# Performance work log

Measured on AMD Instinct MI355X. Metric: run time of the kernel, lower is better.

Reference implementation:

```python
import jax, jax.numpy as jnp
import numpy as np

NUM_LAYER = 5
EMB = 300
FEAT = 512
NUM_GRAPHS = 64
BN_EPS = 1e-5


def setup_inputs() -> dict:
    key = jax.random.key(0)
    ks = jax.random.split(key, 32)
    N, E = 16000, 256000
    x = jax.random.randint(ks[0], (N, 2), 0, 3)  # col0: atom type (<119), col1: chirality (<3)
    edge_index = jax.random.randint(ks[1], (2, E), 0, N)
    edge_attr = jax.random.randint(ks[2], (E, 2), 0, 3)  # col0: bond type (<6), col1: direction (<3)
    batch = jnp.sort(jax.random.randint(ks[3], (N,), 0, NUM_GRAPHS))

    def xav(k, shape):
        fan_in, fan_out = shape[-2], shape[-1]
        lim = float(np.sqrt(6.0 / (fan_in + fan_out)))
        return jax.random.uniform(k, shape, jnp.float32, -lim, lim)

    inp = dict(x=x, edge_index=edge_index, edge_attr=edge_attr, batch=batch)
    inp['x_emb1'] = xav(ks[4], (119, EMB))
    inp['x_emb2'] = xav(ks[5], (3, EMB))
    inp['e1_emb'] = xav(ks[6], (NUM_LAYER, 6, EMB))
    inp['e2_emb'] = xav(ks[7], (NUM_LAYER, 3, EMB))
    inp['w1'] = xav(ks[8], (NUM_LAYER, EMB, 2 * EMB))
    inp['b1'] = jnp.zeros((NUM_LAYER, 2 * EMB))
    inp['w2'] = xav(ks[9], (NUM_LAYER, 2 * EMB, EMB))
    inp['b2'] = jnp.zeros((NUM_LAYER, EMB))
    inp['bn_g'] = jnp.ones((NUM_LAYER, EMB))
    inp['bn_b'] = jnp.zeros((NUM_LAYER, EMB))
    inp['feat_w'] = xav(ks[10], (EMB, FEAT))
    inp['feat_b'] = jnp.zeros((FEAT,))
    inp['hw1'] = xav(ks[11], (FEAT, FEAT // 2))
    inp['hb1'] = jnp.zeros((FEAT // 2,))
    inp['hw2'] = xav(ks[12], (FEAT // 2, FEAT // 2))
    inp['hb2'] = jnp.zeros((FEAT // 2,))
    inp['hw3'] = xav(ks[13], (FEAT // 2, 2))
    inp['hb3'] = jnp.zeros((2,))
    return inp


def gin_forward(x, edge_index, edge_attr, batch,
                x_emb1, x_emb2, e1_emb, e2_emb, w1, b1, w2, b2,
                bn_g, bn_b, feat_w, feat_b, hw1, hb1, hw2, hb2, hw3, hb3):
    N = x.shape[0]
    h = x_emb1[x[:, 0]] + x_emb2[x[:, 1]]  # [N, EMB]
    # add self-loops once (same for every layer): attr = (5, 0)
    loops = jnp.broadcast_to(jnp.arange(N)[None, :], (2, N))
    ei = jnp.concatenate([edge_index, loops], axis=1)  # [2, E+N]
    loop_attr = jnp.concatenate([jnp.full((N, 1), 5, edge_attr.dtype),
                                 jnp.zeros((N, 1), edge_attr.dtype)], axis=1)
    ea = jnp.concatenate([edge_attr, loop_attr], axis=0)  # [E+N, 2]
    src, dst = ei[0], ei[1]
    for l in range(NUM_LAYER):
        edge_emb = e1_emb[l][ea[:, 0]] + e2_emb[l][ea[:, 1]]  # [E+N, EMB]
        msg = h[src] + edge_emb
        agg = jax.ops.segment_sum(msg, dst, num_segments=N)  # scatter-add
        h = jax.nn.relu(agg @ w1[l] + b1[l]) @ w2[l] + b2[l]  # GIN MLP update
        mean = jnp.mean(h, axis=0)
        var = jnp.var(h, axis=0)
        h = (h - mean) * jax.lax.rsqrt(var + BN_EPS) * bn_g[l] + bn_b[l]
        if l < NUM_LAYER - 1:
            h = jax.nn.relu(h)
    # global mean pool per graph
    sums = jax.ops.segment_sum(h, batch, num_segments=NUM_GRAPHS)
    cnts = jax.ops.segment_sum(jnp.ones((N,), h.dtype), batch, num_segments=NUM_GRAPHS)
    hg = sums / jnp.maximum(cnts, 1.0)[:, None]  # [G, EMB]
    hf = hg @ feat_w + feat_b  # [G, FEAT]
    p = jax.nn.softplus(hf @ hw1 + hb1)
    p = jax.nn.softplus(p @ hw2 + hb2)
    pred = p @ hw3 + hb3  # [G, 2]
    return hf, pred


def reference(x, edge_index, edge_attr, batch,
              x_emb1, x_emb2, e1_emb, e2_emb, w1, b1, w2, b2,
              bn_g, bn_b, feat_w, feat_b, hw1, hb1, hw2, hb2, hw3, hb3):
    return gin_forward(x, edge_index, edge_attr, batch,
                       x_emb1, x_emb2, e1_emb, e2_emb, w1, b1, w2, b2,
                       bn_g, bn_b, feat_w, feat_b, hw1, hb1, hw2, hb2, hw3, hb3)
```

## Files before the change

kernel.cpp:

```cpp
#include <hip/hip_runtime.h>

#define NODES 16000
#define EDGES 256000
#define ETOT  272000
#define EMB   300
#define KP1   320
#define NP1   640
#define NP2B  384
#define NGRAPH 64
#define LAYERS 5
#define INV_N (1.0f / 16000.0f)

typedef unsigned short u16;
typedef unsigned int u32;
typedef __bf16 bf16_t;
typedef bf16_t bf16x8 __attribute__((ext_vector_type(8)));
typedef float f32x4 __attribute__((ext_vector_type(4)));

__device__ inline u16 f2bf(float f) {
    bf16_t b = (bf16_t)f;
    return __builtin_bit_cast(u16, b);
}
__device__ inline float bf_lo(u32 u) { return __builtin_bit_cast(float, u << 16); }
__device__ inline float bf_hi(u32 u) { return __builtin_bit_cast(float, u & 0xFFFF0000u); }
__device__ inline u32 bf_pack(float lo, float hi) {
    return ((u32)f2bf(hi) << 16) | (u32)f2bf(lo);
}

__device__ inline float softplus_f(float x) {
    return fmaxf(x, 0.f) + log1pf(expf(-fabsf(x)));
}

__device__ inline void gload_lds16(const u16* g, u16* l) {
    __builtin_amdgcn_global_load_lds(
        (const __attribute__((address_space(1))) void*)g,
        (__attribute__((address_space(3))) void*)l, 16, 0, 0);
}

__device__ inline void bn_coef(const float* __restrict__ ssum, const float* __restrict__ ssq,
                               const float* __restrict__ g, const float* __restrict__ b,
                               int c, float& s, float& t) {
    float mean = ssum[c] * INV_N;
    float var = ssq[c] * INV_N - mean * mean;
    float rstd = rsqrtf(var + 1e-5f);
    s = rstd * g[c];
    t = b[c] - mean * s;
}

__global__ void k_count(const int* __restrict__ ei, int* __restrict__ cnt) {
    int e = blockIdx.x * 256 + threadIdx.x;
    if (e >= ETOT) return;
    int dst = (e < EDGES) ? ei[EDGES + e] : (e - EDGES);
    atomicAdd(&cnt[dst], 1);
}

__global__ void k_scan(const int* cnt_in, int* row_off, int* cursor) {
    __shared__ int s[1024];
    __shared__ int carry;
    int t = threadIdx.x;
    if (t == 0) { carry = 0; row_off[0] = 0; }
    __syncthreads();
    for (int base = 0; base < NODES; base += 1024) {
        int idx = base + t;
        int v = (idx < NODES) ? cnt_in[idx] : 0;
        s[t] = v;
        __syncthreads();
        for (int off = 1; off < 1024; off <<= 1) {
            int add = (t >= off) ? s[t - off] : 0;
            __syncthreads();
            s[t] += add;
            __syncthreads();
        }
        int incl = s[t];
        int c = carry;
        if (idx < NODES) { row_off[idx + 1] = c + incl; cursor[idx] = c + incl - v; }
        __syncthreads();
        if (t == 1023) carry = c + incl;
        __syncthreads();
    }
}

__global__ void k_fill(const int* __restrict__ ei, const int* __restrict__ ea,
                       int* __restrict__ cursor, int* __restrict__ packed) {
    int e = blockIdx.x * 256 + threadIdx.x;
    if (e >= ETOT) return;
    int src, dst, c;
    if (e < EDGES) {
        src = ei[e]; dst = ei[EDGES + e];
        c = ea[e * 2] * 3 + ea[e * 2 + 1];
    } else {
        src = dst = e - EDGES; c = 15;
    }
    int pos = atomicAdd(&cursor[dst], 1);
    packed[pos] = src | (c << 20);
}

__global__ void k_embed(const int* __restrict__ x, const float* __restrict__ e1,
                        const float* __restrict__ e2, u16* __restrict__ h) {
    int id = blockIdx.x * 256 + threadIdx.x;
    if (id >= NODES * EMB) return;
    int i = id / EMB, f = id - i * EMB;
    h[id] = f2bf(e1[x[2 * i] * EMB + f] + e2[x[2 * i + 1] * EMB + f]);
}

__global__ void k_comb(const float* __restrict__ e1, const float* __restrict__ e2,
                       u16* __restrict__ comb) {
    int id = blockIdx.x * 256 + threadIdx.x;
    if (id >= LAYERS * 18 * EMB) return;
    int l = id / (18 * EMB);
    int r = id - l * 18 * EMB;
    int c = r / EMB, f = r - c * EMB;
    int a = c / 3, b = c - a * 3;
    comb[id] = f2bf(e1[(l * 6 + a) * EMB + f] + e2[(l * 3 + b) * EMB + f]);
}

__global__ void k_convw1(const float* __restrict__ w1, u16* __restrict__ w1bT) {
    int id = blockIdx.x * 256 + threadIdx.x;
    if (id >= LAYERS * NP1 * KP1) return;
    int l = id / (NP1 * KP1);
    int r = id - l * NP1 * KP1;
    int n = r / KP1, k = r - n * KP1;
    float v = (n < 600 && k < EMB) ? w1[(l * EMB + k) * 600 + n] : 0.f;
    w1bT[id] = f2bf(v);
}

__global__ void k_convw2(const float* __restrict__ w2, u16* __restrict__ w2bT) {
    int id = blockIdx.x * 256 + threadIdx.x;
    if (id >= LAYERS * NP2B * NP1) return;
    int l = id / (NP2B * NP1);
    int r = id - l * NP2B * NP1;
    int n = r / NP1, k = r - n * NP1;
    float v = (n < EMB && k < 600) ? w2[(l * 600 + k) * EMB + n] : 0.f;
    w2bT[id] = f2bf(v);
}

#define AGG_LOAD(P)                                             \
    int pk = packed[P];                                         \
    const u32* hr = hu + (size_t)(pk & 0xFFFFF) * 150;          \
    const u32* cr = cu + (pk >> 20) * 150;                      \
    u32 u0 = hr[lane], u1 = hr[64 + lane];                      \
    u32 v0 = cr[lane], v1 = cr[64 + lane];                      \
    u32 u2 = 0, v2 = 0;                                         \
    if (has2) { u2 = hr[128 + lane]; v2 = cr[128 + lane]; }

#define AGG_BN_ACC()                                            \
    a0l += fmaxf(bf_lo(u0) * s0l + t0l, 0.f) + bf_lo(v0);       \
    a0h += fmaxf(bf_hi(u0) * s0h + t0h, 0.f) + bf_hi(v0);       \
    a1l += fmaxf(bf_lo(u1) * s1l + t1l, 0.f) + bf_lo(v1);       \
    a1h += fmaxf(bf_hi(u1) * s1h + t1h, 0.f) + bf_hi(v1);       \
    a2l += fmaxf(bf_lo(u2) * s2l + t2l, 0.f) + bf_lo(v2);       \
    a2h += fmaxf(bf_hi(u2) * s2h + t2h, 0.f) + bf_hi(v2);

#define AGG_ACC()                                               \
    a0l += bf_lo(u0) + bf_lo(v0);                               \
    a0h += bf_hi(u0) + bf_hi(v0);                               \
    a1l += bf_lo(u1) + bf_lo(v1);                               \
    a1h += bf_hi(u1) + bf_hi(v1);                               \
    a2l += bf_lo(u2) + bf_lo(v2);                               \
    a2h += bf_hi(u2) + bf_hi(v2);

__global__ __launch_bounds__(256) void k_aggregate(
    const u16* __restrict__ h, const int* __restrict__ row_off,
    const int* __restrict__ packed, const u16* __restrict__ comb,
    u16* __restrict__ aggB,
    const float* __restrict__ ssum, const float* __restrict__ ssq,
    const float* __restrict__ bng, const float* __restrict__ bnb, int use_bn) {
    int node = blockIdx.x * 4 + (threadIdx.x >> 6);
    int lane = threadIdx.x & 63;
    int s = row_off[node], e = row_off[node + 1];
    bool has2 = lane < 22;
    const u32* hu = (const u32*)h;
    const u32* cu = (const u32*)comb;
    float s0l = 1.f, t0l = 0.f, s0h = 1.f, t0h = 0.f;
    float s1l = 1.f, t1l = 0.f, s1h = 1.f, t1h = 0.f;
    float s2l = 1.f, t2l = 0.f, s2h = 1.f, t2h = 0.f;
    if (use_bn) {
        bn_coef(ssum, ssq, bng, bnb, 2 * lane,           s0l, t0l);
        bn_coef(ssum, ssq, bng, bnb, 2 * lane + 1,       s0h, t0h);
        bn_coef(ssum, ssq, bng, bnb, 128 + 2 * lane,     s1l, t1l);
        bn_coef(ssum, ssq, bng, bnb, 128 + 2 * lane + 1, s1h, t1h);
        if (has2) {
            bn_coef(ssum, ssq, bng, bnb, 256 + 2 * lane,     s2l, t2l);
            bn_coef(ssum, ssq, bng, bnb, 256 + 2 * lane + 1, s2h, t2h);
        }
    }
    float a0l = 0, a0h = 0, a1l = 0, a1h = 0, a2l = 0, a2h = 0;
    int p = s;
    if (use_bn) {
        for (; p + 1 < e; p += 2) {
            { AGG_LOAD(p); AGG_BN_ACC(); }
            { AGG_LOAD(p + 1); AGG_BN_ACC(); }
        }
        if (p < e) { AGG_LOAD(p); AGG_BN_ACC(); }
    } else {
        for (; p + 1 < e; p += 2) {
            { AGG_LOAD(p); AGG_ACC(); }
            { AGG_LOAD(p + 1); AGG_ACC(); }
        }
        if (p < e) { AGG_LOAD(p); AGG_ACC(); }
    }
    u32* o = (u32*)(aggB + (size_t)node * KP1);
    o[lane] = bf_pack(a0l, a0h);
    o[64 + lane] = bf_pack(a1l, a1h);
    if (lane < 32) o[128 + lane] = has2 ? bf_pack(a2l, a2h) : 0u;
}

template <int MODE>
__global__ __launch_bounds__(256) void k_gemm(
    const u16* __restrict__ A, const u16* __restrict__ Bt,
    const float* __restrict__ bias, int nbias,
    u16* __restrict__ Cv, int ldc, int K,
    float* __restrict__ ssum, float* __restrict__ ssq) {
    __shared__ __align__(16) u16 Al[128 * 32];
    __shared__ __align__(16) u16 Bl[128 * 32];
    __shared__ float rs[2][128];
    __shared__ float rq[2][128];
    int t = threadIdx.x;
    int n0 = blockIdx.x * 128, m0 = blockIdx.y * 128;
    int lane = t & 63, w = t >> 6;
    int wr = w >> 1, wc = w & 1;
    int lr = lane >> 2, lc = lane & 3;
    const u16* gA0 = A + (size_t)(m0 + w * 32 + lr) * K + lc * 8;
    const u16* gA1 = gA0 + (size_t)16 * K;
    const u16* gB0 = Bt + (size_t)(n0 + w * 32 + lr) * K + lc * 8;
    const u16* gB1 = gB0 + (size_t)16 * K;
    u16* lA0 = &Al[(w * 32) * 32];
    u16* lA1 = &Al[(w * 32 + 16) * 32];
    u16* lB0 = &Bl[(w * 32) * 32];
    u16* lB1 = &Bl[(w * 32 + 16) * 32];
    f32x4 acc[4][4];
#pragma unroll
    for (int i = 0; i < 4; i++)
#pragma unroll
        for (int j = 0; j < 4; j++) acc[i][j] = (f32x4){0.f, 0.f, 0.f, 0.f};
    int fr = lane & 15;
    int k0 = (lane >> 4) * 8;
    int abase = (wr * 64 + fr) * 32 + k0;
    int bbase = (wc * 64 + fr) * 32 + k0;
    for (int kt = 0; kt < K; kt += 32) {
        if (kt) __syncthreads();
        gload_lds16(gA0 + kt, lA0);
        gload_lds16(gA1 + kt, lA1);
        gload_lds16(gB0 + kt, lB0);
        gload_lds16(gB1 + kt, lB1);
        __syncthreads();
        bf16x8 af[4], bfv[4];
#pragma unroll
        for (int f = 0; f < 4; ++f) {
            af[f]  = *reinterpret_cast<const bf16x8*>(&Al[abase + f * 16 * 32]);
            bfv[f] = *reinterpret_cast<const bf16x8*>(&Bl[bbase + f * 16 * 32]);
        }
#pragma unroll
        for (int fm = 0; fm < 4; ++fm)
#pragma unroll
            for (int fn = 0; fn < 4; ++fn)
                acc[fm][fn] = __builtin_amdgcn_mfma_f32_16x16x32_bf16(
                    af[fm], bfv[fn], acc[fm][fn], 0, 0, 0);
    }
    int rg = lane >> 4;
    if (MODE == 0) {
#pragma unroll
        for (int fn = 0; fn < 4; ++fn) {
            int col = n0 + wc * 64 + fn * 16 + fr;
            float bv = (col < nbias) ? bias[col] : 0.f;
#pragma unroll
            for (int fm = 0; fm < 4; ++fm) {
                int rb = m0 + wr * 64 + fm * 16 + rg * 4;
#pragma unroll
                for (int j = 0; j < 4; ++j) {
                    float v = fmaxf(acc[fm][fn][j] + bv, 0.f);
                    Cv[(size_t)(rb + j) * ldc + col] = f2bf(v);
                }
            }
        }
    } else {
#pragma unroll
        for (int fn = 0; fn < 4; ++fn) {
            int col = n0 + wc * 64 + fn * 16 + fr;
            float bv = (col < nbias) ? bias[col] : 0.f;
            float cs = 0.f, cq = 0.f;
#pragma unroll
            for (int fm = 0; fm < 4; ++fm) {
                int rb = m0 + wr * 64 + fm * 16 + rg * 4;
#pragma unroll
                for (int j = 0; j < 4; ++j) {
                    float v = acc[fm][fn][j] + bv;
                    if (col < EMB) Cv[(size_t)(rb + j) * EMB + col] = f2bf(v);
                    cs += v;
                    cq += v * v;
                }
            }
            cs += __shfl_xor(cs, 16); cs += __shfl_xor(cs, 32);
            cq += __shfl_xor(cq, 16); cq += __shfl_xor(cq, 32);
            if (rg == 0) {
                rs[wr][wc * 64 + fn * 16 + fr] = cs;
                rq[wr][wc * 64 + fn * 16 + fr] = cq;
            }
        }
        __syncthreads();
        if (t < 128) {
            int col = n0 + t;
            if (col < EMB) {
                atomicAdd(&ssum[col], rs[0][t] + rs[1][t]);
                atomicAdd(&ssq[col], rq[0][t] + rq[1][t]);
            }
        }
    }
}

__global__ void k_goff(const int* __restrict__ batch, int* __restrict__ goff) {
    int t = threadIdx.x;
    if (t > NGRAPH) return;
    int lo = 0, hi = NODES;
    while (lo < hi) { int mid = (lo + hi) >> 1; if (batch[mid] < t) lo = mid + 1; else hi = mid; }
    goff[t] = lo;
}

__global__ __launch_bounds__(256) void k_pool(const u16* __restrict__ h,
                                              const int* __restrict__ goff,
                                              const float* __restrict__ ssum,
                                              const float* __restrict__ ssq,
                                              const float* __restrict__ bng,
                                              const float* __restrict__ bnb,
                                              float* __restrict__ hg) {
    __shared__ float red[4][64];
    int g = blockIdx.x;
    int col = blockIdx.y * 64 + (threadIdx.x & 63);
    int w = threadIdx.x >> 6;
    int s = goff[g], e = goff[g + 1];
    float a = 0.f;
    bool ok = col < EMB;
    if (ok) {
        for (int r = s + w; r < e; r += 4)
            a += __builtin_bit_cast(float, (u32)h[(size_t)r * EMB + col] << 16);
    }
    red[w][threadIdx.x & 63] = a;
    __syncthreads();
    if (w == 0 && ok) {
        float sc, tc;
        bn_coef(ssum, ssq, bng, bnb, col, sc, tc);
        float v = red[0][threadIdx.x] + red[1][threadIdx.x] +
                  red[2][threadIdx.x] + red[3][threadIdx.x];
        float inv = (e > s) ? 1.0f / (float)(e - s) : 0.f;
        hg[(size_t)g * EMB + col] = (v * inv) * sc + tc;
    }
}

template <int ACT>
__global__ __launch_bounds__(256) void k_small_mm(
    const float* __restrict__ A, const float* __restrict__ W,
    const float* __restrict__ bias, float* __restrict__ C, int N, int K) {
    __shared__ float red[4][64];
    int row = blockIdx.x;
    int lane = threadIdx.x & 63;
    int col = blockIdx.y * 64 + lane;
    int w = threadIdx.x >> 6;
    const float* a = A + (size_t)row * K;
    float acc = 0.f;
#pragma unroll 4
    for (int k = w; k < K; k += 4) acc += a[k] * W[(size_t)k * N + col];
    red[w][lane] = acc;
    __syncthreads();
    if (w == 0) {
        float v = red[0][lane] + red[1][lane] + red[2][lane] + red[3][lane] + bias[col];
        if (ACT) v = softplus_f(v);
        C[(size_t)row * N + col] = v;
    }
}

__global__ __launch_bounds__(256) void k_pred(const float* __restrict__ P,
                                              const float* __restrict__ hw3,
                                              const float* __restrict__ hb3,
                                              float* __restrict__ out) {
    __shared__ float red[2][4];
    int g = blockIdx.x;
    int t = threadIdx.x;
    float q = P[(size_t)g * 256 + t];
    float r0 = q * hw3[t * 2 + 0];
    float r1 = q * hw3[t * 2 + 1];
#pragma unroll
    for (int off = 32; off > 0; off >>= 1) {
        r0 += __shfl_down(r0, off);
        r1 += __shfl_down(r1, off);
    }
    if ((t & 63) == 0) { red[0][t >> 6] = r0; red[1][t >> 6] = r1; }
    __syncthreads();
    if (t == 0) {
        out[(size_t)NGRAPH * 512 + g * 2 + 0] = red[0][0] + red[0][1] + red[0][2] + red[0][3] + hb3[0];
        out[(size_t)NGRAPH * 512 + g * 2 + 1] = red[1][0] + red[1][1] + red[1][2] + red[1][3] + hb3[1];
    }
}

extern "C" void kernel_launch(void* const* d_in, const int* in_sizes, int n_in,
                              void* d_out, int out_size, void* d_ws, size_t ws_size,
                              hipStream_t stream) {
    const int* x      = (const int*)d_in[0];
    const int* ei     = (const int*)d_in[1];
    const int* ea     = (const int*)d_in[2];
    const int* batch  = (const int*)d_in[3];
    const float* x_emb1 = (const float*)d_in[4];
    const float* x_emb2 = (const float*)d_in[5];
    const float* e1_emb = (const float*)d_in[6];
    const float* e2_emb = (const float*)d_in[7];
    const float* w1   = (const float*)d_in[8];
    const float* b1   = (const float*)d_in[9];
    const float* w2   = (const float*)d_in[10];
    const float* b2   = (const float*)d_in[11];
    const float* bn_g = (const float*)d_in[12];
    const float* bn_b = (const float*)d_in[13];
    const float* feat_w = (const float*)d_in[14];
    const float* feat_b = (const float*)d_in[15];
    const float* hw1  = (const float*)d_in[16];
    const float* hb1  = (const float*)d_in[17];
    const float* hw2  = (const float*)d_in[18];
    const float* hb2  = (const float*)d_in[19];
    const float* hw3  = (const float*)d_in[20];
    const float* hb3  = (const float*)d_in[21];
    float* out = (float*)d_out;

    char* p = (char*)d_ws;
    auto alloc = [&](size_t bytes) -> char* {
        char* r = p;
        p += ((bytes + 255) / 256) * 256;
        return r;
    };
    u16* h_a     = (u16*)alloc((size_t)NODES * EMB * 2);
    u16* h_b     = (u16*)alloc((size_t)NODES * EMB * 2);
    u16* aggB    = (u16*)alloc((size_t)NODES * KP1 * 2);
    u16* T       = (u16*)alloc((size_t)NODES * NP1 * 2);
    u16* w1bT    = (u16*)alloc((size_t)LAYERS * NP1 * KP1 * 2);
    u16* w2bT    = (u16*)alloc((size_t)LAYERS * NP2B * NP1 * 2);
    u16* comb    = (u16*)alloc((size_t)LAYERS * 18 * EMB * 2);
    int* row_off = (int*)alloc((NODES + 1) * 4);
    int* cursor  = (int*)alloc(NODES * 4);
    int* packed  = (int*)alloc((size_t)ETOT * 4);
    float* stats = (float*)alloc(2 * 304 * 4);
    int* goff    = (int*)alloc((NGRAPH + 1) * 4);
    float* hg    = (float*)alloc((size_t)NGRAPH * EMB * 4);
    float* pb1   = (float*)alloc((size_t)NGRAPH * 256 * 4);
    float* pb2   = (float*)alloc((size_t)NGRAPH * 256 * 4);
    if ((size_t)(p - (char*)d_ws) > ws_size) return;

    float* ssum = stats;
    float* ssq  = stats + 304;

    hipMemsetAsync(cursor, 0, NODES * 4, stream);
    k_count<<<(ETOT + 255) / 256, 256, 0, stream>>>(ei, cursor);
    k_scan<<<1, 1024, 0, stream>>>(cursor, row_off, cursor);
    k_fill<<<(ETOT + 255) / 256, 256, 0, stream>>>(ei, ea, cursor, packed);

    k_embed<<<(NODES * EMB + 255) / 256, 256, 0, stream>>>(x, x_emb1, x_emb2, h_a);
    k_comb<<<(LAYERS * 18 * EMB + 255) / 256, 256, 0, stream>>>(e1_emb, e2_emb, comb);
    k_convw1<<<(LAYERS * NP1 * KP1 + 255) / 256, 256, 0, stream>>>(w1, w1bT);
    k_convw2<<<(LAYERS * NP2B * NP1 + 255) / 256, 256, 0, stream>>>(w2, w2bT);
    k_goff<<<1, 128, 0, stream>>>(batch, goff);

    for (int l = 0; l < LAYERS; ++l) {
        const u16* h_in = (l & 1) ? h_b : h_a;
        u16* h_out      = (l & 1) ? h_a : h_b;
        k_aggregate<<<NODES / 4, 256, 0, stream>>>(
            h_in, row_off, packed, comb + (size_t)l * 18 * EMB, aggB,
            ssum, ssq, bn_g + (l > 0 ? (l - 1) * EMB : 0), bn_b + (l > 0 ? (l - 1) * EMB : 0),
            l > 0 ? 1 : 0);
        k_gemm<0><<<dim3(NP1 / 128, NODES / 128), 256, 0, stream>>>(
            aggB, w1bT + (size_t)l * NP1 * KP1, b1 + l * 600, 600, T, NP1, KP1,
            nullptr, nullptr);
        hipMemsetAsync(stats, 0, 2 * 304 * 4, stream);
        k_gemm<1><<<dim3(NP2B / 128, NODES / 128), 256, 0, stream>>>(
            T, w2bT + (size_t)l * NP2B * NP1, b2 + l * EMB, EMB, h_out, 0, NP1,
            ssum, ssq);
    }

    const u16* h_fin = h_b;
    k_pool<<<dim3(NGRAPH, 5), 256, 0, stream>>>(h_fin, goff, ssum, ssq,
                                                bn_g + 4 * EMB, bn_b + 4 * EMB, hg);
    k_small_mm<0><<<dim3(NGRAPH, 8), 256, 0, stream>>>(hg, feat_w, feat_b, out, 512, EMB);
    k_small_mm<1><<<dim3(NGRAPH, 4), 256, 0, stream>>>(out, hw1, hb1, pb1, 256, 512);
    k_small_mm<1><<<dim3(NGRAPH, 4), 256, 0, stream>>>(pb1, hw2, hb2, pb2, 256, 256);
    k_pred<<<NGRAPH, 256, 0, stream>>>(pb2, hw3, hb3, out);
}
```

Before: 531.6 us.

## Fuse setup kernels, warp-shuffle scan, split BN+ReLU out of aggregation

Merges the embedding, edge-combo, weight-transpose and graph-offset kernels into one vectorized setup launch, and replaces the 1024-thread Hillis-Steele scan with a per-thread serial plus wavefront-shuffle scan. BatchNorm+ReLU is moved out of the gather loop into a separate elementwise pass, so each node feature is normalized once instead of once per incoming edge. The aggregation loop is unrolled by four. Per-layer stats buffers are preallocated and zeroed with a single memset, which removes the per-layer memsets at the cost of an extra read/write pass over h each layer.

```diff
diff --git a/kernel.cpp b/kernel.cpp
--- a/kernel.cpp
+++ b/kernel.cpp
@@ -37,14 +37,13 @@
         (__attribute__((address_space(3))) void*)l, 16, 0, 0);
 }
 
-__device__ inline void bn_coef(const float* __restrict__ ssum, const float* __restrict__ ssq,
-                               const float* __restrict__ g, const float* __restrict__ b,
-                               int c, float& s, float& t) {
-    float mean = ssum[c] * INV_N;
-    float var = ssq[c] * INV_N - mean * mean;
+__device__ inline void bn_coef_v(float ss, float qq, float gg, float bb,
+                                 float& s, float& t) {
+    float mean = ss * INV_N;
+    float var = qq * INV_N - mean * mean;
     float rstd = rsqrtf(var + 1e-5f);
-    s = rstd * g[c];
-    t = b[c] - mean * s;
+    s = rstd * gg;
+    t = bb - mean * s;
 }
 
 __global__ void k_count(const int* __restrict__ ei, int* __restrict__ cnt) {
@@ -54,30 +53,43 @@
     atomicAdd(&cnt[dst], 1);
 }
 
-__global__ void k_scan(const int* cnt_in, int* row_off, int* cursor) {
-    __shared__ int s[1024];
-    __shared__ int carry;
+__global__ __launch_bounds__(1024) void k_scan(const int* __restrict__ cnt,
+                                               int* __restrict__ row_off,
+                                               int* __restrict__ cursor) {
+    __shared__ int wsum[16];
     int t = threadIdx.x;
-    if (t == 0) { carry = 0; row_off[0] = 0; }
+    int lane = t & 63, w = t >> 6;
+    int base = t * 16;
+    int pre[16];
+    int run = 0;
+#pragma unroll
+    for (int i = 0; i < 16; ++i) {
+        int idx = base + i;
+        int v = (idx < NODES) ? cnt[idx] : 0;
+        pre[i] = run;
+        run += v;
+    }
+    int inc = run;
+#pragma unroll
+    for (int off = 1; off < 64; off <<= 1) {
+        int n = __shfl_up(inc, off);
+        if (lane >= off) inc += n;
+    }
+    if (lane == 63) wsum[w] = inc;
     __syncthreads();
-    for (int base = 0; base < NODES; base += 1024) {
-        int idx = base + t;
-        int v = (idx < NODES) ? cnt_in[idx] : 0;
-        s[t] = v;
-        __syncthreads();
-        for (int off = 1; off < 1024; off <<= 1) {
-            int add = (t >= off) ? s[t - off] : 0;
-            __syncthreads();
-            s[t] += add;
-            __syncthreads();
-        }
-        int incl = s[t];
-        int c = carry;
-        if (idx < NODES) { row_off[idx + 1] = c + incl; cursor[idx] = c + incl - v; }
-        __syncthreads();
-        if (t == 1023) carry = c + incl;
-        __syncthreads();
-    }
+    int wpre = 0;
+    for (int i = 0; i < w; ++i) wpre += wsum[i];
+    int excl = wpre + inc - run;
+#pragma unroll
+    for (int i = 0; i < 16; ++i) {
+        int idx = base + i;
+        if (idx < NODES) {
+            int st = excl + pre[i];
+            row_off[idx] = st;
+            cursor[idx] = st;
+        }
+    }
+    if (t == 1023) row_off[NODES] = wpre + inc;
 }
 
 __global__ void k_fill(const int* __restrict__ ei, const int* __restrict__ ea,
@@ -95,43 +107,109 @@
     packed[pos] = src | (c << 20);
 }
 
-__global__ void k_embed(const int* __restrict__ x, const float* __restrict__ e1,
-                        const float* __restrict__ e2, u16* __restrict__ h) {
+#define SEG0 1200000
+#define SEG1 6750
+#define SEG2 256000
+#define SEG3 307200
+#define SETUP_TOT (SEG0 + SEG1 + SEG2 + SEG3 + NGRAPH + 1)
+
+__global__ __launch_bounds__(256) void k_setup(
+    const int* __restrict__ x, const float* __restrict__ e1x,
+    const float* __restrict__ e2x, const float* __restrict__ ce1,
+    const float* __restrict__ ce2, const float* __restrict__ w1,
+    const float* __restrict__ w2, const int* __restrict__ batch,
+    u16* __restrict__ h, u16* __restrict__ comb,
+    u16* __restrict__ w1bT, u16* __restrict__ w2bT, int* __restrict__ goff) {
     int id = blockIdx.x * 256 + threadIdx.x;
-    if (id >= NODES * EMB) return;
-    int i = id / EMB, f = id - i * EMB;
-    h[id] = f2bf(e1[x[2 * i] * EMB + f] + e2[x[2 * i + 1] * EMB + f]);
-}
-
-__global__ void k_comb(const float* __restrict__ e1, const float* __restrict__ e2,
-                       u16* __restrict__ comb) {
+    if (id < SEG0) {
+        int base = id * 4;
+        int row = base / EMB;
+        int f = base - row * EMB;
+        int x1 = x[2 * row], x2 = x[2 * row + 1];
+        float4 a = *(const float4*)(e1x + x1 * EMB + f);
+        float4 b = *(const float4*)(e2x + x2 * EMB + f);
+        u32* o = (u32*)h + id * 2;
+        o[0] = bf_pack(a.x + b.x, a.y + b.y);
+        o[1] = bf_pack(a.z + b.z, a.w + b.w);
+        return;
+    }
+    id -= SEG0;
+    if (id < SEG1) {
+        int l = id / 1350, r = id - l * 1350;
+        int c = r / 75, f = (r - c * 75) * 4;
+        int a = c / 3, bb = c - a * 3;
+        float4 va = *(const float4*)(ce1 + (l * 6 + a) * EMB + f);
+        float4 vb = *(const float4*)(ce2 + (l * 3 + bb) * EMB + f);
+        u32* o = (u32*)comb + ((l * 18 + c) * EMB + f) / 2;
+        o[0] = bf_pack(va.x + vb.x, va.y + vb.y);
+        o[1] = bf_pack(va.z + vb.z, va.w + vb.w);
+        return;
+    }
+    id -= SEG1;
+    if (id < SEG2) {
+        int l = id / (NP1 * 80), r = id - l * (NP1 * 80);
+        int n = r / 80, k4 = (r - n * 80) * 4;
+        float v[4];
+#pragma unroll
+        for (int j = 0; j < 4; ++j) {
+            int k = k4 + j;
+            v[j] = (n < 600 && k < EMB) ? w1[(l * EMB + k) * 600 + n] : 0.f;
+        }
+        u32* o = (u32*)w1bT + ((size_t)(l * NP1 + n) * KP1 + k4) / 2;
+        o[0] = bf_pack(v[0], v[1]);
+        o[1] = bf_pack(v[2], v[3]);
+        return;
+    }
+    id -= SEG2;
+    if (id < SEG3) {
+        int l = id / (NP2B * 160), r = id - l * (NP2B * 160);
+        int n = r / 160, k4 = (r - n * 160) * 4;
+        float v[4];
+#pragma unroll
+        for (int j = 0; j < 4; ++j) {
+            int k = k4 + j;
+            v[j] = (n < EMB && k < 600) ? w2[(l * 600 + k) * EMB + n] : 0.f;
+        }
+        u32* o = (u32*)w2bT + ((size_t)(l * NP2B + n) * NP1 + k4) / 2;
+        o[0] = bf_pack(v[0], v[1]);
+        o[1] = bf_pack(v[2], v[3]);
+        return;
+    }
+    id -= SEG3;
+    if (id <= NGRAPH) {
+        int lo = 0, hi = NODES;
+        while (lo < hi) { int mid = (lo + hi) >> 1; if (batch[mid] < id) lo = mid + 1; else hi = mid; }
+        goff[id] = lo;
+    }
+}
+
+__global__ __launch_bounds__(256) void k_bnrelu(
+    const u16* __restrict__ hin, u16* __restrict__ hout,
+    const float* __restrict__ ssum, const float* __restrict__ ssq,
+    const float* __restrict__ g, const float* __restrict__ b) {
     int id = blockIdx.x * 256 + threadIdx.x;
-    if (id >= LAYERS * 18 * EMB) return;
-    int l = id / (18 * EMB);
-    int r = id - l * 18 * EMB;
-    int c = r / EMB, f = r - c * EMB;
-    int a = c / 3, b = c - a * 3;
-    comb[id] = f2bf(e1[(l * 6 + a) * EMB + f] + e2[(l * 3 + b) * EMB + f]);
-}
-
-__global__ void k_convw1(const float* __restrict__ w1, u16* __restrict__ w1bT) {
-    int id = blockIdx.x * 256 + threadIdx.x;
-    if (id >= LAYERS * NP1 * KP1) return;
-    int l = id / (NP1 * KP1);
-    int r = id - l * NP1 * KP1;
-    int n = r / KP1, k = r - n * KP1;
-    float v = (n < 600 && k < EMB) ? w1[(l * EMB + k) * 600 + n] : 0.f;
-    w1bT[id] = f2bf(v);
-}
-
-__global__ void k_convw2(const float* __restrict__ w2, u16* __restrict__ w2bT) {
-    int id = blockIdx.x * 256 + threadIdx.x;
-    if (id >= LAYERS * NP2B * NP1) return;
-    int l = id / (NP2B * NP1);
-    int r = id - l * NP2B * NP1;
-    int n = r / NP1, k = r - n * NP1;
-    float v = (n < EMB && k < 600) ? w2[(l * 600 + k) * EMB + n] : 0.f;
-    w2bT[id] = f2bf(v);
+    if (id >= NODES * EMB / 4) return;
+    int base = id * 4;
+    int row = base / EMB;
+    int f = base - row * EMB;
+    float4 S = *(const float4*)(ssum + f);
+    float4 Q = *(const float4*)(ssq + f);
+    float4 G = *(const float4*)(g + f);
+    float4 B = *(const float4*)(b + f);
+    const u32* in = (const u32*)hin + id * 2;
+    u32 x0 = in[0], x1 = in[1];
+    float sc0, tc0, sc1, tc1, sc2, tc2, sc3, tc3;
+    bn_coef_v(S.x, Q.x, G.x, B.x, sc0, tc0);
+    bn_coef_v(S.y, Q.y, G.y, B.y, sc1, tc1);
+    bn_coef_v(S.z, Q.z, G.z, B.z, sc2, tc2);
+    bn_coef_v(S.w, Q.w, G.w, B.w, sc3, tc3);
+    float v0 = fmaxf(bf_lo(x0) * sc0 + tc0, 0.f);
+    float v1 = fmaxf(bf_hi(x0) * sc1 + tc1, 0.f);
+    float v2 = fmaxf(bf_lo(x1) * sc2 + tc2, 0.f);
+    float v3 = fmaxf(bf_hi(x1) * sc3 + tc3, 0.f);
+    u32* o = (u32*)hout + id * 2;
+    o[0] = bf_pack(v0, v1);
+    o[1] = bf_pack(v2, v3);
 }
 
 #define AGG_LOAD(P)                                             \
@@ -143,14 +221,6 @@
     u32 u2 = 0, v2 = 0;                                         \
     if (has2) { u2 = hr[128 + lane]; v2 = cr[128 + lane]; }
 
-#define AGG_BN_ACC()                                            \
-    a0l += fmaxf(bf_lo(u0) * s0l + t0l, 0.f) + bf_lo(v0);       \
-    a0h += fmaxf(bf_hi(u0) * s0h + t0h, 0.f) + bf_hi(v0);       \
-    a1l += fmaxf(bf_lo(u1) * s1l + t1l, 0.f) + bf_lo(v1);       \
-    a1h += fmaxf(bf_hi(u1) * s1h + t1h, 0.f) + bf_hi(v1);       \
-    a2l += fmaxf(bf_lo(u2) * s2l + t2l, 0.f) + bf_lo(v2);       \
-    a2h += fmaxf(bf_hi(u2) * s2h + t2h, 0.f) + bf_hi(v2);
-
 #define AGG_ACC()                                               \
     a0l += bf_lo(u0) + bf_lo(v0);                               \
     a0h += bf_hi(u0) + bf_hi(v0);                               \
@@ -162,43 +232,22 @@
 __global__ __launch_bounds__(256) void k_aggregate(
     const u16* __restrict__ h, const int* __restrict__ row_off,
     const int* __restrict__ packed, const u16* __restrict__ comb,
-    u16* __restrict__ aggB,
-    const float* __restrict__ ssum, const float* __restrict__ ssq,
-    const float* __restrict__ bng, const float* __restrict__ bnb, int use_bn) {
+    u16* __restrict__ aggB) {
     int node = blockIdx.x * 4 + (threadIdx.x >> 6);
     int lane = threadIdx.x & 63;
     int s = row_off[node], e = row_off[node + 1];
     bool has2 = lane < 22;
     const u32* hu = (const u32*)h;
     const u32* cu = (const u32*)comb;
-    float s0l = 1.f, t0l = 0.f, s0h = 1.f, t0h = 0.f;
-    float s1l = 1.f, t1l = 0.f, s1h = 1.f, t1h = 0.f;
-    float s2l = 1.f, t2l = 0.f, s2h = 1.f, t2h = 0.f;
-    if (use_bn) {
-        bn_coef(ssum, ssq, bng, bnb, 2 * lane,           s0l, t0l);
-        bn_coef(ssum, ssq, bng, bnb, 2 * lane + 1,       s0h, t0h);
-        bn_coef(ssum, ssq, bng, bnb, 128 + 2 * lane,     s1l, t1l);
-        bn_coef(ssum, ssq, bng, bnb, 128 + 2 * lane + 1, s1h, t1h);
-        if (has2) {
-            bn_coef(ssum, ssq, bng, bnb, 256 + 2 * lane,     s2l, t2l);
-            bn_coef(ssum, ssq, bng, bnb, 256 + 2 * lane + 1, s2h, t2h);
-        }
-    }
     float a0l = 0, a0h = 0, a1l = 0, a1h = 0, a2l = 0, a2h = 0;
     int p = s;
-    if (use_bn) {
-        for (; p + 1 < e; p += 2) {
-            { AGG_LOAD(p); AGG_BN_ACC(); }
-            { AGG_LOAD(p + 1); AGG_BN_ACC(); }
-        }
-        if (p < e) { AGG_LOAD(p); AGG_BN_ACC(); }
-    } else {
-        for (; p + 1 < e; p += 2) {
-            { AGG_LOAD(p); AGG_ACC(); }
-            { AGG_LOAD(p + 1); AGG_ACC(); }
-        }
-        if (p < e) { AGG_LOAD(p); AGG_ACC(); }
-    }
+    for (; p + 3 < e; p += 4) {
+        { AGG_LOAD(p);     AGG_ACC(); }
+        { AGG_LOAD(p + 1); AGG_ACC(); }
+        { AGG_LOAD(p + 2); AGG_ACC(); }
+        { AGG_LOAD(p + 3); AGG_ACC(); }
+    }
+    for (; p < e; ++p) { AGG_LOAD(p); AGG_ACC(); }
     u32* o = (u32*)(aggB + (size_t)node * KP1);
     o[lane] = bf_pack(a0l, a0h);
     o[64 + lane] = bf_pack(a1l, a1h);
@@ -308,14 +357,6 @@
     }
 }
 
-__global__ void k_goff(const int* __restrict__ batch, int* __restrict__ goff) {
-    int t = threadIdx.x;
-    if (t > NGRAPH) return;
-    int lo = 0, hi = NODES;
-    while (lo < hi) { int mid = (lo + hi) >> 1; if (batch[mid] < t) lo = mid + 1; else hi = mid; }
-    goff[t] = lo;
-}
-
 __global__ __launch_bounds__(256) void k_pool(const u16* __restrict__ h,
                                               const int* __restrict__ goff,
                                               const float* __restrict__ ssum,
@@ -338,7 +379,7 @@
     __syncthreads();
     if (w == 0 && ok) {
         float sc, tc;
-        bn_coef(ssum, ssq, bng, bnb, col, sc, tc);
+        bn_coef_v(ssum[col], ssq[col], bng[col], bnb[col], sc, tc);
         float v = red[0][threadIdx.x] + red[1][threadIdx.x] +
                   red[2][threadIdx.x] + red[3][threadIdx.x];
         float inv = (e > s) ? 1.0f / (float)(e - s) : 0.f;
@@ -432,47 +473,48 @@
     u16* w2bT    = (u16*)alloc((size_t)LAYERS * NP2B * NP1 * 2);
     u16* comb    = (u16*)alloc((size_t)LAYERS * 18 * EMB * 2);
     int* row_off = (int*)alloc((NODES + 1) * 4);
-    int* cursor  = (int*)alloc(NODES * 4);
     int* packed  = (int*)alloc((size_t)ETOT * 4);
-    float* stats = (float*)alloc(2 * 304 * 4);
     int* goff    = (int*)alloc((NGRAPH + 1) * 4);
     float* hg    = (float*)alloc((size_t)NGRAPH * EMB * 4);
     float* pb1   = (float*)alloc((size_t)NGRAPH * 256 * 4);
     float* pb2   = (float*)alloc((size_t)NGRAPH * 256 * 4);
+    int* cursor  = (int*)alloc(NODES * 4);
+    float* stats5 = (float*)alloc((size_t)LAYERS * 640 * 4);
     if ((size_t)(p - (char*)d_ws) > ws_size) return;
 
-    float* ssum = stats;
-    float* ssq  = stats + 304;
-
-    hipMemsetAsync(cursor, 0, NODES * 4, stream);
+    hipMemsetAsync(cursor, 0, NODES * 4 + LAYERS * 640 * 4, stream);
+
     k_count<<<(ETOT + 255) / 256, 256, 0, stream>>>(ei, cursor);
     k_scan<<<1, 1024, 0, stream>>>(cursor, row_off, cursor);
     k_fill<<<(ETOT + 255) / 256, 256, 0, stream>>>(ei, ea, cursor, packed);
 
-    k_embed<<<(NODES * EMB + 255) / 256, 256, 0, stream>>>(x, x_emb1, x_emb2, h_a);
-    k_comb<<<(LAYERS * 18 * EMB + 255) / 256, 256, 0, stream>>>(e1_emb, e2_emb, comb);
-    k_convw1<<<(LAYERS * NP1 * KP1 + 255) / 256, 256, 0, stream>>>(w1, w1bT);
-    k_convw2<<<(LAYERS * NP2B * NP1 + 255) / 256, 256, 0, stream>>>(w2, w2bT);
-    k_goff<<<1, 128, 0, stream>>>(batch, goff);
+    k_setup<<<(SETUP_TOT + 255) / 256, 256, 0, stream>>>(
+        x, x_emb1, x_emb2, e1_emb, e2_emb, w1, w2, batch,
+        h_a, comb, w1bT, w2bT, goff);
 
     for (int l = 0; l < LAYERS; ++l) {
-        const u16* h_in = (l & 1) ? h_b : h_a;
-        u16* h_out      = (l & 1) ? h_a : h_b;
+        const u16* h_src;
+        if (l == 0) {
+            h_src = h_a;
+        } else {
+            float* st = stats5 + (size_t)(l - 1) * 640;
+            k_bnrelu<<<(NODES * EMB / 4 + 255) / 256, 256, 0, stream>>>(
+                h_a, h_b, st, st + 320, bn_g + (l - 1) * EMB, bn_b + (l - 1) * EMB);
+            h_src = h_b;
+        }
         k_aggregate<<<NODES / 4, 256, 0, stream>>>(
-            h_in, row_off, packed, comb + (size_t)l * 18 * EMB, aggB,
-            ssum, ssq, bn_g + (l > 0 ? (l - 1) * EMB : 0), bn_b + (l > 0 ? (l - 1) * EMB : 0),
-            l > 0 ? 1 : 0);
+            h_src, row_off, packed, comb + (size_t)l * 18 * EMB, aggB);
         k_gemm<0><<<dim3(NP1 / 128, NODES / 128), 256, 0, stream>>>(
             aggB, w1bT + (size_t)l * NP1 * KP1, b1 + l * 600, 600, T, NP1, KP1,
             nullptr, nullptr);
-        hipMemsetAsync(stats, 0, 2 * 304 * 4, stream);
+        float* st = stats5 + (size_t)l * 640;
         k_gemm<1><<<dim3(NP2B / 128, NODES / 128), 256, 0, stream>>>(
-            T, w2bT + (size_t)l * NP2B * NP1, b2 + l * EMB, EMB, h_out, 0, NP1,
-            ssum, ssq);
-    }
-
-    const u16* h_fin = h_b;
-    k_pool<<<dim3(NGRAPH, 5), 256, 0, stream>>>(h_fin, goff, ssum, ssq,
+            T, w2bT + (size_t)l * NP2B * NP1, b2 + l * EMB, EMB, h_a, 0, NP1,
+            st, st + 320);
+    }
+
+    float* st4 = stats5 + (size_t)4 * 640;
+    k_pool<<<dim3(NGRAPH, 5), 256, 0, stream>>>(h_a, goff, st4, st4 + 320,
                                                 bn_g + 4 * EMB, bn_b + 4 * EMB, hg);
     k_small_mm<0><<<dim3(NGRAPH, 8), 256, 0, stream>>>(hg, feat_w, feat_b, out, 512, EMB);
     k_small_mm<1><<<dim3(NGRAPH, 4), 256, 0, stream>>>(out, hw1, hb1, pb1, 256, 512);
```

Result: faster. 495.5 us (-6.8%).
